# Optimization experiments

Hardware: AMD Instinct MI355X
Metric: run time of the kernel (lower is better)

Reference implementation:

```python
import jax, jax.numpy as jnp
import numpy as np

NH, NL, NPNT = 8, 4, 4          # heads, levels, points
NQ, BS, NK, D, DFFN = 100, 8, 18, 256, 1024
SPATIAL = np.array([[92, 92], [46, 46], [23, 23], [12, 12]], np.int32)
LEN_MEM = int((SPATIAL[:, 0] * SPATIAL[:, 1]).sum())  # 11253


def _layernorm(x, g, b):
    m = x.mean(-1, keepdims=True)
    v = ((x - m) ** 2).mean(-1, keepdims=True)
    return (x - m) / jnp.sqrt(v + 1e-5) * g + b


def _mha(xq, xk, xv, in_w, in_b, out_w, out_b):
    # torch nn.MultiheadAttention semantics, inputs (S, B, D)
    S, B, d = xq.shape
    dh = d // NH
    wq, wk, wv = jnp.split(in_w, 3, axis=0)
    bq, bk, bv = jnp.split(in_b, 3, axis=0)
    def proj(x, w, b):
        return (x @ w.T + b).reshape(x.shape[0], B, NH, dh).transpose(1, 2, 0, 3)
    q = proj(xq, wq, bq) * (1.0 / np.sqrt(dh))
    k = proj(xk, wk, bk)
    v = proj(xv, wv, bv)
    att = jax.nn.softmax(jnp.einsum('bhqd,bhkd->bhqk', q, k), axis=-1)
    o = jnp.einsum('bhqk,bhkd->bhqd', att, v).transpose(2, 0, 1, 3).reshape(S, B, d)
    return o @ out_w.T + out_b


def _bilinear(v_l, loc):
    # v_l: (bs,H,W,NH,dh); loc: (bs,Lq,NH,P,2) normalized [0,1]
    # matches F.grid_sample(align_corners=False, padding_mode='zeros')
    bs, H, W, nh, dh = v_l.shape
    x = loc[..., 0] * W - 0.5
    y = loc[..., 1] * H - 0.5
    x0 = jnp.floor(x); y0 = jnp.floor(y)
    lx = x - x0; ly = y - y0
    b_idx = jnp.arange(bs)[:, None, None, None]
    h_idx = jnp.arange(nh)[None, None, :, None]
    def corner(xa, ya, w):
        valid = (xa >= 0) & (xa < W) & (ya >= 0) & (ya < H)
        xi = jnp.clip(xa, 0, W - 1).astype(jnp.int32)
        yi = jnp.clip(ya, 0, H - 1).astype(jnp.int32)
        return v_l[b_idx, yi, xi, h_idx] * (w * valid)[..., None]
    return (corner(x0, y0, (1 - lx) * (1 - ly)) + corner(x0 + 1, y0, lx * (1 - ly))
            + corner(x0, y0 + 1, (1 - lx) * ly) + corner(x0 + 1, y0 + 1, lx * ly))


def _msda(q, rp, mem, pad_mask, ss, off_w, off_b, aw_w, aw_b, val_w, val_b, outp_w, outp_b):
    bs, Lq, d = q.shape
    dh = d // NH
    value = mem @ val_w.T + val_b
    value = jnp.where(pad_mask[..., None], 0.0, value).reshape(bs, -1, NH, dh)
    off = (q @ off_w.T + off_b).reshape(bs, Lq, NH, NL, NPNT, 2)
    aw = jax.nn.softmax((q @ aw_w.T + aw_b).reshape(bs, Lq, NH, NL * NPNT), -1)
    aw = aw.reshape(bs, Lq, NH, NL, NPNT)
    wh = jnp.asarray(ss[:, ::-1].copy(), jnp.float32)  # offset normalizer (W, H)
    loc = rp[:, :, None, :, None, :] + off / wh[None, None, None, :, None, :]
    out = jnp.zeros((bs, Lq, NH, dh), q.dtype)
    start = 0
    for l in range(NL):
        H, W = int(ss[l, 0]), int(ss[l, 1])
        v_l = value[:, start:start + H * W].reshape(bs, H, W, NH, dh)
        start += H * W
        samp = _bilinear(v_l, loc[:, :, :, l])          # (bs,Lq,NH,P,dh)
        out = out + (samp * aw[:, :, :, l, :, None]).sum(3)
    return out.reshape(bs, Lq, d) @ outp_w.T + outp_b


def _forward(tgt_pose, pos, ref_points, memory, w_in_w, w_in_b, w_out_w, w_out_b,
             a_in_w, a_in_b, a_out_w, a_out_b, off_w, off_b, aw_w, aw_b,
             val_w, val_b, outp_w, outp_b, wn_g, wn_b, an_g, an_b,
             n1_g, n1_b, n2_g, n2_b, l1_w, l1_b, l2_w, l2_b,
             spatial_shapes, level_start_index, padding_mask):
    ss = np.asarray(jax.device_get(spatial_shapes))
    nq, bs, nk, d = tgt_pose.shape
    # within-group self-attn over the nk keypoint tokens.
    # NOTE: with_pos_embed mutates tgt_pose in place in the torch code, so
    # q = k = v = tgt + pos and the residual also uses tgt + pos (faithful).
    t = tgt_pose + pos
    x = t.reshape(nq * bs, nk, d).transpose(1, 0, 2)   # (nk, nq*bs, d)
    a1 = _mha(x, x, x, w_in_w, w_in_b, w_out_w, w_out_b)
    t = _layernorm(t + a1.transpose(1, 0, 2).reshape(nq, bs, nk, d), wn_g, wn_b)
    # across-group self-attn over the nq groups
    x2 = t.reshape(nq, bs * nk, d)
    a2 = _mha(x2, x2, x2, a_in_w, a_in_b, a_out_w, a_out_b)
    t = _layernorm(t + a2.reshape(nq, bs, nk, d), an_g, an_b)
    # MSDeformAttn cross-attention (in-place pos add again, faithful)
    t = t + pos
    q = t.transpose(1, 0, 2, 3).reshape(bs, nq * nk, d)
    rp = jnp.swapaxes(ref_points, 0, 1)                # (bs, nq*nk, NL, 2)
    mem = jnp.swapaxes(memory, 0, 1)                   # (bs, LEN_MEM, d)
    c = _msda(q, rp, mem, padding_mask, ss, off_w, off_b, aw_w, aw_b,
              val_w, val_b, outp_w, outp_b)
    c = c.reshape(bs, nq, nk, d).transpose(1, 0, 2, 3)
    t = _layernorm(t + c, n1_g, n1_b)
    # FFN (dropout is identity in eval)
    h = jax.nn.relu(t @ l1_w.T + l1_b)
    return _layernorm(t + (h @ l2_w.T + l2_b), n2_g, n2_b)


def setup_inputs() -> dict:
    key = jax.random.key(0)
    ks = jax.random.split(key, 16)
    p = lambda k, shape: jax.random.normal(k, shape, jnp.float32) * 0.02
    lsi = np.concatenate([[0], np.cumsum(SPATIAL[:, 0] * SPATIAL[:, 1])[:-1]]).astype(np.int32)
    return {
        'tgt_pose': jax.random.normal(ks[0], (NQ, BS, NK, D), jnp.float32),
        'pos': jax.random.normal(ks[1], (NQ, BS, NK, D), jnp.float32),
        'ref_points': jax.random.uniform(ks[2], (NQ * NK, BS, NL, 2), jnp.float32),
        'memory': jax.random.normal(ks[3], (LEN_MEM, BS, D), jnp.float32),
        'w_in_w': p(ks[4], (3 * D, D)), 'w_in_b': jnp.zeros((3 * D,)),
        'w_out_w': p(ks[5], (D, D)), 'w_out_b': jnp.zeros((D,)),
        'a_in_w': p(ks[6], (3 * D, D)), 'a_in_b': jnp.zeros((3 * D,)),
        'a_out_w': p(ks[7], (D, D)), 'a_out_b': jnp.zeros((D,)),
        'off_w': p(ks[8], (NH * NL * NPNT * 2, D)),
        'off_b': jax.random.uniform(ks[9], (NH * NL * NPNT * 2,), jnp.float32, -2.0, 2.0),
        'aw_w': p(ks[10], (NH * NL * NPNT, D)), 'aw_b': jnp.zeros((NH * NL * NPNT,)),
        'val_w': p(ks[11], (D, D)), 'val_b': jnp.zeros((D,)),
        'outp_w': p(ks[12], (D, D)), 'outp_b': jnp.zeros((D,)),
        'wn_g': jnp.ones((D,)), 'wn_b': jnp.zeros((D,)),
        'an_g': jnp.ones((D,)), 'an_b': jnp.zeros((D,)),
        'n1_g': jnp.ones((D,)), 'n1_b': jnp.zeros((D,)),
        'n2_g': jnp.ones((D,)), 'n2_b': jnp.zeros((D,)),
        'l1_w': p(ks[13], (DFFN, D)), 'l1_b': jnp.zeros((DFFN,)),
        'l2_w': p(ks[14], (D, DFFN)), 'l2_b': jnp.zeros((D,)),
        'spatial_shapes': jnp.asarray(SPATIAL),
        'level_start_index': jnp.asarray(lsi),
        'padding_mask': jnp.zeros((BS, LEN_MEM), bool),
    }


def reference(tgt_pose, pos, ref_points, memory, w_in_w, w_in_b, w_out_w, w_out_b,
              a_in_w, a_in_b, a_out_w, a_out_b, off_w, off_b, aw_w, aw_b,
              val_w, val_b, outp_w, outp_b, wn_g, wn_b, an_g, an_b,
              n1_g, n1_b, n2_g, n2_b, l1_w, l1_b, l2_w, l2_b,
              spatial_shapes, level_start_index, padding_mask):
    return _forward(tgt_pose, pos, ref_points, memory, w_in_w, w_in_b, w_out_w, w_out_b,
                    a_in_w, a_in_b, a_out_w, a_out_b, off_w, off_b, aw_w, aw_b,
                    val_w, val_b, outp_w, outp_b, wn_g, wn_b, an_g, an_b,
                    n1_g, n1_b, n2_g, n2_b, l1_w, l1_b, l2_w, l2_b,
                    spatial_shapes, level_start_index, padding_mask)
```

## Files before the change

kernel.cpp:

```cpp
#include <hip/hip_runtime.h>
#include <math.h>

#define NH_ 8
#define D_ 256
#define NK_ 18
#define NQ_ 100
#define BS_ 8
#define LQ_ 1800
#define LEN_MEM_ 11253
#define NTOK_ 14400

typedef short bf16x8 __attribute__((ext_vector_type(8)));
typedef float f32x4 __attribute__((ext_vector_type(4)));
typedef unsigned short ushort;

__device__ inline ushort f2bf(float f) {
    unsigned int u = __builtin_bit_cast(unsigned int, f);
    unsigned int r = (u + 0x7fffu + ((u >> 16) & 1u)) >> 16;
    return (ushort)r;
}
__device__ inline float bf2f(unsigned int u16) {
    unsigned int i = u16 << 16;
    return __builtin_bit_cast(float, i);
}
__device__ inline float bf2f_hi(unsigned int u) {
    unsigned int i = u & 0xffff0000u;
    return __builtin_bit_cast(float, i);
}
__device__ inline float bf2f_lo(unsigned int u) {
    unsigned int i = u << 16;
    return __builtin_bit_cast(float, i);
}
__device__ inline int packbf2(float a, float b) {
    return (int)f2bf(a) | ((int)f2bf(b) << 16);
}

__global__ __launch_bounds__(256)
void wcvt_kernel(const float* s0, const float* s1, const float* s2, const float* s3,
                 const float* s4, const float* s5, const float* s6, const float* s7,
                 const float* s8, const float* s9, ushort* dst) {
    const int sizes[10] = {196608,65536,196608,65536,65536,32768,65536,65536,262144,262144};
    const int offs[10]  = {0,196608,262144,458752,524288,589824,622592,688128,753664,1015808};
    int ti = blockIdx.y;
    const float* s;
    switch (ti) {
        case 0: s = s0; break; case 1: s = s1; break; case 2: s = s2; break;
        case 3: s = s3; break; case 4: s = s4; break; case 5: s = s5; break;
        case 6: s = s6; break; case 7: s = s7; break; case 8: s = s8; break;
        default: s = s9; break;
    }
    int n = sizes[ti];
    int i = (blockIdx.x * 256 + threadIdx.x) * 8;
    if (i >= n) return;
    ushort* d = dst + offs[ti] + i;
    float4 f0 = *(const float4*)(s + i);
    float4 f1 = *(const float4*)(s + i + 4);
    int4 val;
    val.x = packbf2(f0.x, f0.y);
    val.y = packbf2(f0.z, f0.w);
    val.z = packbf2(f1.x, f1.y);
    val.w = packbf2(f1.z, f1.w);
    *(int4*)d = val;
}

__global__ __launch_bounds__(256)
void addcvt_kernel(const float* __restrict__ a, const float* __restrict__ b,
                   float* __restrict__ c, ushort* __restrict__ cbf, int n4) {
    int i = blockIdx.x * blockDim.x + threadIdx.x;
    if (i >= n4) return;
    float4 av = ((const float4*)a)[i];
    float4 bv = ((const float4*)b)[i];
    float4 cv;
    cv.x = av.x + bv.x; cv.y = av.y + bv.y; cv.z = av.z + bv.z; cv.w = av.w + bv.w;
    ((float4*)c)[i] = cv;
    uint2 p;
    p.x = (unsigned int)packbf2(cv.x, cv.y);
    p.y = (unsigned int)packbf2(cv.z, cv.w);
    *(uint2*)(cbf + (size_t)i * 4) = p;
}

template<int MODE, bool RELU, bool A_F32, bool OUT_BF16, int BN, int WAVES, int R>
__global__ __launch_bounds__(WAVES * 64)
void gemmw_kernel(const void* __restrict__ Av, const ushort* __restrict__ W,
                  const float* __restrict__ bias, void* __restrict__ Cv,
                  int M, int N, const unsigned char* __restrict__ mask) {
    constexpr int K = 256;
    constexpr int NT = BN / 16;
    __shared__ ushort Ws[32 * BN * 8];
    const int tid = threadIdx.x;
    const int m0 = blockIdx.x * (WAVES * 16 * R);
    const int n0 = blockIdx.y * BN;

    for (int c = tid; c < 32 * BN; c += WAVES * 64) {
        int kc = c & 31, n = c >> 5;
        int dst = kc * BN + (n ^ (kc & 7));
        *(int4*)(Ws + dst * 8) = *(const int4*)(W + (long)(n0 + n) * K + kc * 8);
    }
    __syncthreads();

    const int wv = tid >> 6, lane = tid & 63, fr = lane & 15, hi = lane >> 4;
    const int wm0 = m0 + wv * (16 * R);
    long arow[R];
#pragma unroll
    for (int r = 0; r < R; ++r) {
        int gr = wm0 + r * 16 + fr;
        if (gr > M - 1) gr = M - 1;
        if (MODE == 2) {
            int b = gr / LQ_; int lq = gr - b * LQ_;
            int q = lq / NK_; int kk = lq - q * NK_;
            arow[r] = (long)q * (BS_ * NK_) + b * NK_ + kk;
        } else {
            arow[r] = gr;
        }
    }

    f32x4 acc[R][NT];
#pragma unroll
    for (int r = 0; r < R; ++r)
#pragma unroll
        for (int t = 0; t < NT; ++t) acc[r][t] = f32x4{0.f, 0.f, 0.f, 0.f};

    if (A_F32) {
        const float* ap[R];
        float4 p0[R], p1[R];
#pragma unroll
        for (int r = 0; r < R; ++r) {
            ap[r] = (const float*)Av + arow[r] * (long)K + hi * 8;
            p0[r] = *(const float4*)ap[r];
            p1[r] = *(const float4*)(ap[r] + 4);
        }
#pragma unroll
        for (int ks = 0; ks < 8; ++ks) {
            bf16x8 cur[R];
#pragma unroll
            for (int r = 0; r < R; ++r) {
                int4 v;
                v.x = packbf2(p0[r].x, p0[r].y); v.y = packbf2(p0[r].z, p0[r].w);
                v.z = packbf2(p1[r].x, p1[r].y); v.w = packbf2(p1[r].z, p1[r].w);
                cur[r] = __builtin_bit_cast(bf16x8, v);
                if (ks < 7) {
                    p0[r] = *(const float4*)(ap[r] + (ks + 1) * 32);
                    p1[r] = *(const float4*)(ap[r] + (ks + 1) * 32 + 4);
                }
            }
            const int kc = ks * 4 + hi;
            const ushort* wb = Ws + ((kc * BN) + (fr ^ (kc & 7))) * 8;
#pragma unroll
            for (int t = 0; t < NT; ++t) {
                bf16x8 wf = *(const bf16x8*)(wb + t * 128);
#pragma unroll
                for (int r = 0; r < R; ++r)
                    acc[r][t] = __builtin_amdgcn_mfma_f32_16x16x32_bf16(cur[r], wf, acc[r][t], 0, 0, 0);
            }
        }
    } else {
        const ushort* ap[R];
        bf16x8 afrag[R];
#pragma unroll
        for (int r = 0; r < R; ++r) {
            ap[r] = (const ushort*)Av + arow[r] * (long)K + hi * 8;
            afrag[r] = *(const bf16x8*)ap[r];
        }
#pragma unroll
        for (int ks = 0; ks < 8; ++ks) {
            bf16x8 cur[R];
#pragma unroll
            for (int r = 0; r < R; ++r) {
                cur[r] = afrag[r];
                if (ks < 7) afrag[r] = *(const bf16x8*)(ap[r] + (ks + 1) * 32);
            }
            const int kc = ks * 4 + hi;
            const ushort* wb = Ws + ((kc * BN) + (fr ^ (kc & 7))) * 8;
#pragma unroll
            for (int t = 0; t < NT; ++t) {
                bf16x8 wf = *(const bf16x8*)(wb + t * 128);
#pragma unroll
                for (int r = 0; r < R; ++r)
                    acc[r][t] = __builtin_amdgcn_mfma_f32_16x16x32_bf16(cur[r], wf, acc[r][t], 0, 0, 0);
            }
        }
    }

#pragma unroll
    for (int r = 0; r < R; ++r) {
#pragma unroll
        for (int rr = 0; rr < 4; ++rr) {
            int gm = wm0 + r * 16 + hi * 4 + rr;
            if (gm >= M) continue;
            long orow = gm;
            bool zero = false;
            if (MODE == 1) {
                if (mask && mask[(size_t)(gm & 7) * LEN_MEM_ + (gm >> 3)]) zero = true;
            } else if (MODE == 3) {
                int b = gm / LQ_; int lq = gm - b * LQ_;
                int q = lq / NK_; int kk = lq - q * NK_;
                orow = (long)q * (BS_ * NK_) + b * NK_ + kk;
            }
#pragma unroll
            for (int t = 0; t < NT; ++t) {
                int gn = n0 + t * 16 + fr;
                float v = acc[r][t][rr] + bias[gn];
                if (RELU) v = fmaxf(v, 0.f);
                if (zero) v = 0.f;
                if (OUT_BF16) ((ushort*)Cv)[orow * (long)N + gn] = f2bf(v);
                else ((float*)Cv)[orow * (long)N + gn] = v;
            }
        }
    }
}

template<int MODE, bool RELU, bool A_F32, bool OUT_BF16>
__global__ __launch_bounds__(256)
void gemm_kernel(const void* __restrict__ Av, const ushort* __restrict__ W,
                 const float* __restrict__ bias, void* __restrict__ Cv,
                 int M, int N, int K, const unsigned char* __restrict__ mask) {
    constexpr int AST = 72;
    __shared__ ushort As[128 * AST];
    __shared__ ushort Bs[128 * AST];
    const int m0 = blockIdx.x * 128, n0 = blockIdx.y * 128;
    const int tid = threadIdx.x;
    const int w = tid >> 6, lane = tid & 63;
    const int wr = w >> 1, wc = w & 1;
    const int fr = lane & 15, hi = lane >> 4;
    f32x4 acc[4][4];
#pragma unroll
    for (int i = 0; i < 4; ++i)
#pragma unroll
        for (int j = 0; j < 4; ++j) acc[i][j] = f32x4{0.f, 0.f, 0.f, 0.f};

    const int srow = tid >> 1, shalf = tid & 1;
    long arow = 0;
    const bool avalid = (m0 + srow) < M;
    {
        int gr = m0 + srow;
        if (gr >= M) gr = M - 1;
        arow = gr;
    }

    for (int k0 = 0; k0 < K; k0 += 64) {
        ushort* ad = As + srow * AST + shalf * 32;
        if (avalid) {
            const ushort* ap = (const ushort*)Av + arow * (long)K + k0 + shalf * 32;
#pragma unroll
            for (int i = 0; i < 4; ++i) *(int4*)(ad + i * 8) = *(const int4*)(ap + i * 8);
        } else {
            int4 z = make_int4(0, 0, 0, 0);
#pragma unroll
            for (int i = 0; i < 4; ++i) *(int4*)(ad + i * 8) = z;
        }
        {
            const ushort* wp = W + (long)(n0 + srow) * K + k0 + shalf * 32;
            ushort* bd = Bs + srow * AST + shalf * 32;
#pragma unroll
            for (int i = 0; i < 4; ++i) *(int4*)(bd + i * 8) = *(const int4*)(wp + i * 8);
        }
        __syncthreads();
#pragma unroll
        for (int kb = 0; kb < 2; ++kb) {
            bf16x8 af[4], bfr[4];
#pragma unroll
            for (int i = 0; i < 4; ++i)
                af[i] = *(const bf16x8*)(As + (wr * 64 + i * 16 + fr) * AST + kb * 32 + hi * 8);
#pragma unroll
            for (int j = 0; j < 4; ++j)
                bfr[j] = *(const bf16x8*)(Bs + (wc * 64 + j * 16 + fr) * AST + kb * 32 + hi * 8);
#pragma unroll
            for (int i = 0; i < 4; ++i)
#pragma unroll
                for (int j = 0; j < 4; ++j)
                    acc[i][j] = __builtin_amdgcn_mfma_f32_16x16x32_bf16(af[i], bfr[j], acc[i][j], 0, 0, 0);
        }
        __syncthreads();
    }

#pragma unroll
    for (int i = 0; i < 4; ++i) {
#pragma unroll
        for (int r = 0; r < 4; ++r) {
            int gm = m0 + wr * 64 + i * 16 + hi * 4 + r;
            if (gm >= M) continue;
#pragma unroll
            for (int j = 0; j < 4; ++j) {
                int gn = n0 + wc * 64 + j * 16 + fr;
                float v = acc[i][j][r] + bias[gn];
                if (RELU) v = fmaxf(v, 0.f);
                if (OUT_BF16) ((ushort*)Cv)[(long)gm * N + gn] = f2bf(v);
                else ((float*)Cv)[(long)gm * N + gn] = v;
            }
        }
    }
}

template<int S, int SP, int HPB>
__global__ __launch_bounds__(256)
void mattn_kernel(const ushort* __restrict__ qkv, ushort* __restrict__ outb,
                  int rsG, int rsS) {
    constexpr int SPk = ((SP + 31) / 32) * 32;
    constexpr int KST = 40;
    constexpr int PST = SPk + 8;
    constexpr int NT = SP / 16;
    constexpr int NB = HPB * NT;
    constexpr int HB = 8 / HPB;
    __shared__ ushort KsA[HPB * SP * KST];
    __shared__ ushort VtA[HPB * 32 * PST];
    __shared__ ushort PA [HPB * SP * PST];

    const int tid = threadIdx.x;
    const int g = blockIdx.x / HB;
    const int hbase = (blockIdx.x % HB) * HPB;

    for (int idx = tid; idx < HPB * S * 4; idx += 256) {
        int hh = idx / (S * 4); int rem = idx - hh * (S * 4);
        int j = rem >> 2, q = rem & 3;
        const ushort* base = qkv + ((size_t)g * rsG + (size_t)j * rsS) * 768 + (hbase + hh) * 32 + q * 8;
        uint4 kv = *(const uint4*)(base + 256);
        ushort* kd = KsA + hh * (SP * KST) + j * KST + q * 8;
        *(uint2*)kd = make_uint2(kv.x, kv.y);
        *(uint2*)(kd + 4) = make_uint2(kv.z, kv.w);
        uint4 vv = *(const uint4*)(base + 512);
        ushort* vt = VtA + hh * (32 * PST) + j;
        unsigned int uu[4] = {vv.x, vv.y, vv.z, vv.w};
#pragma unroll
        for (int e = 0; e < 4; ++e) {
            vt[(q * 8 + e * 2    ) * PST] = (ushort)(uu[e] & 0xffff);
            vt[(q * 8 + e * 2 + 1) * PST] = (ushort)(uu[e] >> 16);
        }
    }
    for (int idx = tid; idx < HPB * 32 * (SPk - S); idx += 256) {
        int hh = idx / (32 * (SPk - S)); int rem = idx - hh * (32 * (SPk - S));
        int d = rem / (SPk - S); int c = S + rem - d * (SPk - S);
        VtA[hh * 32 * PST + d * PST + c] = 0;
    }
    if constexpr (SPk > SP) {
        constexpr int PW = SPk - SP;
        for (int idx = tid; idx < HPB * SP * PW; idx += 256) {
            int hh = idx / (SP * PW); int rem = idx - hh * (SP * PW);
            int rrow = rem / PW; int c = SP + rem - rrow * PW;
            PA[hh * SP * PST + rrow * PST + c] = 0;
        }
    }
    __syncthreads();

    const int wv = tid >> 6, lane = tid & 63, fr = lane & 15, hi = lane >> 4;
    for (int band = wv; band < NB; band += 4) {
        const int hh = band / NT, mb = band - (band / NT) * NT;
        const int h = hbase + hh;
        const ushort* Ks = KsA + hh * (SP * KST);
        const ushort* Vt = VtA + hh * (32 * PST);
        ushort* P = PA + hh * (SP * PST);

        int sq = mb * 16 + fr; if (sq > S - 1) sq = S - 1;
        bf16x8 qf = *(const bf16x8*)(qkv + ((size_t)g * rsG + (size_t)sq * rsS) * 768 + h * 32 + hi * 8);
        f32x4 sc[NT];
#pragma unroll
        for (int t = 0; t < NT; ++t) {
            bf16x8 kf = *(const bf16x8*)(Ks + (t * 16 + fr) * KST + hi * 8);
            sc[t] = __builtin_amdgcn_mfma_f32_16x16x32_bf16(qf, kf, f32x4{0.f, 0.f, 0.f, 0.f}, 0, 0, 0);
        }
#pragma unroll
        for (int t = 0; t < NT; ++t) {
            bool valid = (t * 16 + fr) < S;
#pragma unroll
            for (int r = 0; r < 4; ++r)
                sc[t][r] = valid ? sc[t][r] * 0.17677669529663687f : -1e30f;
        }
#pragma unroll
        for (int r = 0; r < 4; ++r) {
            float m = sc[0][r];
#pragma unroll
            for (int t = 1; t < NT; ++t) m = fmaxf(m, sc[t][r]);
            m = fmaxf(m, __shfl_xor(m, 1)); m = fmaxf(m, __shfl_xor(m, 2));
            m = fmaxf(m, __shfl_xor(m, 4)); m = fmaxf(m, __shfl_xor(m, 8));
            float e[NT]; float sum = 0.f;
#pragma unroll
            for (int t = 0; t < NT; ++t) { e[t] = __expf(sc[t][r] - m); sum += e[t]; }
            sum += __shfl_xor(sum, 1); sum += __shfl_xor(sum, 2);
            sum += __shfl_xor(sum, 4); sum += __shfl_xor(sum, 8);
            float inv = 1.f / sum;
            int row = mb * 16 + hi * 4 + r;
#pragma unroll
            for (int t = 0; t < NT; ++t)
                P[row * PST + t * 16 + fr] = f2bf(e[t] * inv);
        }
        f32x4 o0 = {0.f, 0.f, 0.f, 0.f}, o1 = {0.f, 0.f, 0.f, 0.f};
#pragma unroll
        for (int kb = 0; kb < SPk / 32; ++kb) {
            bf16x8 pf = *(const bf16x8*)(P + (mb * 16 + fr) * PST + kb * 32 + hi * 8);
            bf16x8 v0 = *(const bf16x8*)(Vt + fr * PST + kb * 32 + hi * 8);
            bf16x8 v1 = *(const bf16x8*)(Vt + (16 + fr) * PST + kb * 32 + hi * 8);
            o0 = __builtin_amdgcn_mfma_f32_16x16x32_bf16(pf, v0, o0, 0, 0, 0);
            o1 = __builtin_amdgcn_mfma_f32_16x16x32_bf16(pf, v1, o1, 0, 0, 0);
        }
#pragma unroll
        for (int r = 0; r < 4; ++r) {
            int s = mb * 16 + hi * 4 + r;
            if (s < S) {
                size_t ob = ((size_t)g * rsG + (size_t)s * rsS) * 256 + h * 32;
                outb[ob + fr] = f2bf(o0[r]);
                outb[ob + 16 + fr] = f2bf(o1[r]);
            }
        }
    }
}

__global__ __launch_bounds__(256)
void addln_kernel(const float* __restrict__ base, const float* __restrict__ delta,
                  const float* __restrict__ gamma, const float* __restrict__ beta,
                  const float* __restrict__ pos,
                  float* __restrict__ out, ushort* __restrict__ obf, int M) {
    int row = blockIdx.x * 4 + (threadIdx.x >> 6);
    int lane = threadIdx.x & 63;
    if (row >= M) return;
    const float* pb = base + (size_t)row * 256;
    const float* pd = delta + (size_t)row * 256;
    float v[4]; float s = 0.f;
#pragma unroll
    for (int i = 0; i < 4; ++i) { int c = lane + i * 64; v[i] = pb[c] + pd[c]; s += v[i]; }
#pragma unroll
    for (int off = 32; off; off >>= 1) s += __shfl_xor(s, off);
    float mean = s * (1.f / 256.f);
    float var = 0.f;
#pragma unroll
    for (int i = 0; i < 4; ++i) { float d = v[i] - mean; var += d * d; }
#pragma unroll
    for (int off = 32; off; off >>= 1) var += __shfl_xor(var, off);
    var *= (1.f / 256.f);
    float rstd = rsqrtf(var + 1e-5f);
#pragma unroll
    for (int i = 0; i < 4; ++i) {
        int c = lane + i * 64;
        float o = (v[i] - mean) * rstd * gamma[c] + beta[c];
        if (pos) o += pos[(size_t)row * 256 + c];
        out[(size_t)row * 256 + c] = o;
        if (obf) obf[(size_t)row * 256 + c] = f2bf(o);
    }
}

__global__ __launch_bounds__(256)
void msda_kernel(const float* __restrict__ offb, const float* __restrict__ aw,
                 const ushort* __restrict__ val, const float* __restrict__ refp,
                 const int* __restrict__ spatial, const int* __restrict__ lsi,
                 ushort* __restrict__ samp) {
    const int unit = blockIdx.x * 64 + (threadIdx.x >> 2);
    const int lane4 = threadIdx.x & 3;
    const int base = (threadIdx.x & 63) & 60;
    const int h = unit & 7;
    const int t = unit >> 3;
    const int lq = t % LQ_;
    const int b = t / LQ_;
    const size_t row = (size_t)b * LQ_ + lq;

    float4 lg = *(const float4*)(aw + row * 128 + h * 16 + lane4 * 4);
    float m = fmaxf(fmaxf(lg.x, lg.y), fmaxf(lg.z, lg.w));
    m = fmaxf(m, __shfl_xor(m, 1)); m = fmaxf(m, __shfl_xor(m, 2));
    float4 e;
    e.x = __expf(lg.x - m); e.y = __expf(lg.y - m);
    e.z = __expf(lg.z - m); e.w = __expf(lg.w - m);
    float s = e.x + e.y + e.z + e.w;
    s += __shfl_xor(s, 1); s += __shfl_xor(s, 2);
    float inv = 1.f / s;
    float4 w4; w4.x = e.x * inv; w4.y = e.y * inv; w4.z = e.z * inv; w4.w = e.w * inv;

    const float* offp = offb + row * 256 + h * 32;
    float4 oA = *(const float4*)(offp + lane4 * 8);
    float4 oB = *(const float4*)(offp + lane4 * 8 + 4);

    float acc[8];
#pragma unroll
    for (int c = 0; c < 8; ++c) acc[c] = 0.f;

#pragma unroll
    for (int lvl = 0; lvl < 4; ++lvl) {
        int H = spatial[lvl * 2], W = spatial[lvl * 2 + 1];
        int st = lsi[lvl];
        float rpx = refp[(((size_t)lq * BS_ + b) * 4 + lvl) * 2 + 0];
        float rpy = refp[(((size_t)lq * BS_ + b) * 4 + lvl) * 2 + 1];
        const ushort* vb = val + ((size_t)st * 8 + b) * 256 + h * 32 + lane4 * 8;
        float fW = (float)W, fH = (float)H;
#pragma unroll
        for (int p = 0; p < 4; ++p) {
            const int pi = lvl * 4 + p;
            const int j = pi >> 2, q = pi & 3;
            float ox_, oy_, wp_;
            if (q == 0)      { ox_ = oA.x; oy_ = oA.y; wp_ = w4.x; }
            else if (q == 1) { ox_ = oA.z; oy_ = oA.w; wp_ = w4.y; }
            else if (q == 2) { ox_ = oB.x; oy_ = oB.y; wp_ = w4.z; }
            else             { ox_ = oB.z; oy_ = oB.w; wp_ = w4.w; }
            float ox  = __shfl(ox_, base + j);
            float oy  = __shfl(oy_, base + j);
            float wpt = __shfl(wp_, base + j);

            float x = rpx * fW + ox - 0.5f;
            float y = rpy * fH + oy - 0.5f;
            float x0f = floorf(x), y0f = floorf(y);
            float lx = x - x0f, ly = y - y0f;
            int x0 = (int)x0f, y0 = (int)y0f;
            int xc0 = min(max(x0, 0), W - 1), xc1 = min(max(x0 + 1, 0), W - 1);
            int yc0 = min(max(y0, 0), H - 1), yc1 = min(max(y0 + 1, 0), H - 1);
            float vx0 = (x0 >= 0 && x0 < W) ? 1.f : 0.f;
            float vx1 = (x0 >= -1 && x0 + 1 < W) ? 1.f : 0.f;
            float vy0 = (y0 >= 0 && y0 < H) ? 1.f : 0.f;
            float vy1 = (y0 >= -1 && y0 + 1 < H) ? 1.f : 0.f;
            float w00 = wpt * (1.f - lx) * (1.f - ly) * vx0 * vy0;
            float w10 = wpt * lx * (1.f - ly) * vx1 * vy0;
            float w01 = wpt * (1.f - lx) * ly * vx0 * vy1;
            float w11 = wpt * lx * ly * vx1 * vy1;
            uint4 u00 = *(const uint4*)(vb + (size_t)(yc0 * W + xc0) * 2048);
            uint4 u10 = *(const uint4*)(vb + (size_t)(yc0 * W + xc1) * 2048);
            uint4 u01 = *(const uint4*)(vb + (size_t)(yc1 * W + xc0) * 2048);
            uint4 u11 = *(const uint4*)(vb + (size_t)(yc1 * W + xc1) * 2048);
            const unsigned int* a00 = (const unsigned int*)&u00;
            const unsigned int* a10 = (const unsigned int*)&u10;
            const unsigned int* a01 = (const unsigned int*)&u01;
            const unsigned int* a11 = (const unsigned int*)&u11;
#pragma unroll
            for (int k = 0; k < 4; ++k) {
                acc[2 * k]     += w00 * bf2f_lo(a00[k]) + w10 * bf2f_lo(a10[k])
                                + w01 * bf2f_lo(a01[k]) + w11 * bf2f_lo(a11[k]);
                acc[2 * k + 1] += w00 * bf2f_hi(a00[k]) + w10 * bf2f_hi(a10[k])
                                + w01 * bf2f_hi(a01[k]) + w11 * bf2f_hi(a11[k]);
            }
        }
    }
    size_t o = row * 256 + h * 32 + lane4 * 8;
    uint4 pk;
    pk.x = (unsigned int)packbf2(acc[0], acc[1]);
    pk.y = (unsigned int)packbf2(acc[2], acc[3]);
    pk.z = (unsigned int)packbf2(acc[4], acc[5]);
    pk.w = (unsigned int)packbf2(acc[6], acc[7]);
    *(uint4*)(samp + o) = pk;
}

extern "C" void kernel_launch(void* const* d_in, const int* in_sizes, int n_in,
                              void* d_out, int out_size, void* d_ws, size_t ws_size,
                              hipStream_t stream) {
    const float* tgt     = (const float*)d_in[0];
    const float* pos     = (const float*)d_in[1];
    const float* refp    = (const float*)d_in[2];
    const float* memory  = (const float*)d_in[3];
    const float* w_in_w  = (const float*)d_in[4];
    const float* w_in_b  = (const float*)d_in[5];
    const float* w_out_w = (const float*)d_in[6];
    const float* w_out_b = (const float*)d_in[7];
    const float* a_in_w  = (const float*)d_in[8];
    const float* a_in_b  = (const float*)d_in[9];
    const float* a_out_w = (const float*)d_in[10];
    const float* a_out_b = (const float*)d_in[11];
    const float* off_w   = (const float*)d_in[12];
    const float* off_b   = (const float*)d_in[13];
    const float* aw_w    = (const float*)d_in[14];
    const float* aw_b    = (const float*)d_in[15];
    const float* val_w   = (const float*)d_in[16];
    const float* val_b   = (const float*)d_in[17];
    const float* outp_w  = (const float*)d_in[18];
    const float* outp_b  = (const float*)d_in[19];
    const float* wn_g    = (const float*)d_in[20];
    const float* wn_b    = (const float*)d_in[21];
    const float* an_g    = (const float*)d_in[22];
    const float* an_b    = (const float*)d_in[23];
    const float* n1_g    = (const float*)d_in[24];
    const float* n1_b    = (const float*)d_in[25];
    const float* n2_g    = (const float*)d_in[26];
    const float* n2_b    = (const float*)d_in[27];
    const float* l1_w    = (const float*)d_in[28];
    const float* l1_b    = (const float*)d_in[29];
    const float* l2_w    = (const float*)d_in[30];
    const float* l2_b    = (const float*)d_in[31];
    const int*   spatial = (const int*)d_in[32];
    const int*   lsi     = (const int*)d_in[33];
    const unsigned char* pmask = (const unsigned char*)d_in[34];
    float* out = (float*)d_out;

    float*  T      = (float*)d_ws;
    ushort* Tbf    = (ushort*)(T + 3686400);
    ushort* B16    = Tbf + 3686400;
    ushort* CBbf   = B16 + 11059200;
    ushort* VALbf  = CBbf + 3686400;
    ushort* SAMPbf = VALbf + 23046144;
    ushort* Hbf    = SAMPbf + 3686400;
    ushort* WB     = Hbf + 14745600;
    float*  OFF    = (float*)(WB + 1277952);
    float*  AW     = OFF + 3686400;

    ushort* WB_win  = WB + 0;
    ushort* WB_wout = WB + 196608;
    ushort* WB_ain  = WB + 262144;
    ushort* WB_aout = WB + 458752;
    ushort* WB_off  = WB + 524288;
    ushort* WB_aw   = WB + 589824;
    ushort* WB_val  = WB + 622592;
    ushort* WB_outp = WB + 688128;
    ushort* WB_l1   = WB + 753664;
    ushort* WB_l2   = WB + 1015808;

    const int n4 = NTOK_ * 256 / 4;

    wcvt_kernel<<<dim3(128, 10), 256, 0, stream>>>(
        w_in_w, w_out_w, a_in_w, a_out_w, off_w, aw_w, val_w, outp_w, l1_w, l2_w, WB);
    addcvt_kernel<<<n4 / 256, 256, 0, stream>>>(tgt, pos, T, Tbf, n4);
    gemmw_kernel<0, false, false, true, 64, 4, 2><<<dim3(113, 12), 256, 0, stream>>>(
        Tbf, WB_win, w_in_b, B16, NTOK_, 768, nullptr);
    mattn_kernel<18, 32, 4><<<800 * 2, 256, 0, stream>>>(B16, CBbf, 18, 1);
    gemmw_kernel<0, false, false, false, 64, 4, 2><<<dim3(113, 4), 256, 0, stream>>>(
        CBbf, WB_wout, w_out_b, OFF, NTOK_, 256, nullptr);
    addln_kernel<<<NTOK_ / 4, 256, 0, stream>>>(T, OFF, wn_g, wn_b, nullptr, T, Tbf, NTOK_);
    gemmw_kernel<0, false, false, true, 64, 4, 2><<<dim3(113, 12), 256, 0, stream>>>(
        Tbf, WB_ain, a_in_b, B16, NTOK_, 768, nullptr);
    mattn_kernel<100, 112, 1><<<144 * 8, 256, 0, stream>>>(B16, CBbf, 1, 144);
    gemmw_kernel<0, false, false, false, 64, 4, 2><<<dim3(113, 4), 256, 0, stream>>>(
        CBbf, WB_aout, a_out_b, OFF, NTOK_, 256, nullptr);
    addln_kernel<<<NTOK_ / 4, 256, 0, stream>>>(T, OFF, an_g, an_b, pos, T, Tbf, NTOK_);
    gemmw_kernel<1, false, true, true, 128, 8, 2><<<dim3(352, 2), 512, 0, stream>>>(
        memory, WB_val, val_b, VALbf, 90024, 256, pmask);
    gemmw_kernel<2, false, false, false, 64, 4, 2><<<dim3(113, 4), 256, 0, stream>>>(
        Tbf, WB_off, off_b, OFF, NTOK_, 256, nullptr);
    gemmw_kernel<2, false, false, false, 64, 4, 2><<<dim3(113, 2), 256, 0, stream>>>(
        Tbf, WB_aw, aw_b, AW, NTOK_, 128, nullptr);
    msda_kernel<<<1800, 256, 0, stream>>>(OFF, AW, VALbf, refp, spatial, lsi, SAMPbf);
    gemmw_kernel<3, false, false, false, 64, 4, 2><<<dim3(113, 4), 256, 0, stream>>>(
        SAMPbf, WB_outp, outp_b, OFF, NTOK_, 256, nullptr);
    addln_kernel<<<NTOK_ / 4, 256, 0, stream>>>(T, OFF, n1_g, n1_b, nullptr, T, Tbf, NTOK_);
    gemmw_kernel<0, true, false, true, 64, 4, 2><<<dim3(113, 16), 256, 0, stream>>>(
        Tbf, WB_l1, l1_b, Hbf, NTOK_, 1024, nullptr);
    gemm_kernel<0, false, false, false><<<dim3(113, 2), 256, 0, stream>>>(
        Hbf, WB_l2, l2_b, OFF, NTOK_, 256, 1024, nullptr);
    addln_kernel<<<NTOK_ / 4, 256, 0, stream>>>(T, OFF, n2_g, n2_b, nullptr, out, nullptr, NTOK_);
}
```

Measured before the change: 359.6 us.

## Stage fp32 value-projection A tile through LDS with coalesced loads

Adds a dedicated value-projection GEMM that loads a 128-row fp32 memory tile with fully coalesced float4 reads, converts it to bf16 once, and stores it swizzled in LDS before the MFMA loop. It replaces the previous path where each lane streamed strided fp32 fragments straight from global memory, and removes the now-unused fp32-A branch from the generic GEMM. It is aimed at the memory-bound value projection over 90k rows. In exchange it uses more LDS per block (about 128 KB), which limits occupancy to one block per CU, and it launches twice as many blocks with one row tile per wave.

```diff
diff --git a/kernel.cpp b/kernel.cpp
--- a/kernel.cpp
+++ b/kernel.cpp
@@ -79,6 +79,74 @@
     *(uint2*)(cbf + (size_t)i * 4) = p;
 }
 
+__global__ __launch_bounds__(512)
+void gemmv_kernel(const float* __restrict__ A, const ushort* __restrict__ W,
+                  const float* __restrict__ bias, ushort* __restrict__ C,
+                  int M, int N, const unsigned char* __restrict__ mask) {
+    constexpr int K = 256;
+    constexpr int BN = 128;
+    __shared__ ushort Ws[32 * BN * 8];
+    __shared__ ushort As[32 * 128 * 8];
+    const int tid = threadIdx.x;
+    const int m0 = blockIdx.x * 128;
+    const int n0 = blockIdx.y * BN;
+
+    for (int c = tid; c < 32 * BN; c += 512) {
+        int kc = c & 31, n = c >> 5;
+        int dst = kc * BN + (n ^ (kc & 7));
+        *(int4*)(Ws + dst * 8) = *(const int4*)(W + (long)(n0 + n) * K + kc * 8);
+    }
+    {
+        const float4* src = (const float4*)(A + (size_t)m0 * K);
+#pragma unroll
+        for (int s = 0; s < 16; ++s) {
+            int p4 = s * 512 + tid;
+            int row = p4 >> 6;
+            int p4r = (m0 + row < M) ? p4 : (p4 & 63);
+            float4 f = src[p4r];
+            int k8 = (p4 >> 1) & 31, half = p4 & 1;
+            uint2 v;
+            v.x = (unsigned int)packbf2(f.x, f.y);
+            v.y = (unsigned int)packbf2(f.z, f.w);
+            *(uint2*)(As + (k8 * 128 + (row ^ (k8 & 7))) * 8 + half * 4) = v;
+        }
+    }
+    __syncthreads();
+
+    const int wv = tid >> 6, lane = tid & 63, fr = lane & 15, hi = lane >> 4;
+    const int rowl = wv * 16 + fr;
+
+    f32x4 acc[8];
+#pragma unroll
+    for (int t = 0; t < 8; ++t) acc[t] = f32x4{0.f, 0.f, 0.f, 0.f};
+
+#pragma unroll
+    for (int ks = 0; ks < 8; ++ks) {
+        const int kc = ks * 4 + hi;
+        bf16x8 af = *(const bf16x8*)(As + (kc * 128 + (rowl ^ (kc & 7))) * 8);
+        const ushort* wb = Ws + ((kc * BN) + (fr ^ (kc & 7))) * 8;
+#pragma unroll
+        for (int t = 0; t < 8; ++t) {
+            bf16x8 wf = *(const bf16x8*)(wb + t * 128);
+            acc[t] = __builtin_amdgcn_mfma_f32_16x16x32_bf16(af, wf, acc[t], 0, 0, 0);
+        }
+    }
+
+#pragma unroll
+    for (int rr = 0; rr < 4; ++rr) {
+        int gm = m0 + wv * 16 + hi * 4 + rr;
+        if (gm >= M) continue;
+        bool zero = mask && mask[(size_t)(gm & 7) * LEN_MEM_ + (gm >> 3)];
+#pragma unroll
+        for (int t = 0; t < 8; ++t) {
+            int gn = n0 + t * 16 + fr;
+            float v = acc[t][rr] + bias[gn];
+            if (zero) v = 0.f;
+            C[(long)gm * N + gn] = f2bf(v);
+        }
+    }
+}
+
 template<int MODE, bool RELU, bool A_F32, bool OUT_BF16, int BN, int WAVES, int R>
 __global__ __launch_bounds__(WAVES * 64)
 void gemmw_kernel(const void* __restrict__ Av, const ushort* __restrict__ W,
@@ -120,40 +188,7 @@
 #pragma unroll
         for (int t = 0; t < NT; ++t) acc[r][t] = f32x4{0.f, 0.f, 0.f, 0.f};
 
-    if (A_F32) {
-        const float* ap[R];
-        float4 p0[R], p1[R];
-#pragma unroll
-        for (int r = 0; r < R; ++r) {
-            ap[r] = (const float*)Av + arow[r] * (long)K + hi * 8;
-            p0[r] = *(const float4*)ap[r];
-            p1[r] = *(const float4*)(ap[r] + 4);
-        }
-#pragma unroll
-        for (int ks = 0; ks < 8; ++ks) {
-            bf16x8 cur[R];
-#pragma unroll
-            for (int r = 0; r < R; ++r) {
-                int4 v;
-                v.x = packbf2(p0[r].x, p0[r].y); v.y = packbf2(p0[r].z, p0[r].w);
-                v.z = packbf2(p1[r].x, p1[r].y); v.w = packbf2(p1[r].z, p1[r].w);
-                cur[r] = __builtin_bit_cast(bf16x8, v);
-                if (ks < 7) {
-                    p0[r] = *(const float4*)(ap[r] + (ks + 1) * 32);
-                    p1[r] = *(const float4*)(ap[r] + (ks + 1) * 32 + 4);
-                }
-            }
-            const int kc = ks * 4 + hi;
-            const ushort* wb = Ws + ((kc * BN) + (fr ^ (kc & 7))) * 8;
-#pragma unroll
-            for (int t = 0; t < NT; ++t) {
-                bf16x8 wf = *(const bf16x8*)(wb + t * 128);
-#pragma unroll
-                for (int r = 0; r < R; ++r)
-                    acc[r][t] = __builtin_amdgcn_mfma_f32_16x16x32_bf16(cur[r], wf, acc[r][t], 0, 0, 0);
-            }
-        }
-    } else {
+    {
         const ushort* ap[R];
         bf16x8 afrag[R];
 #pragma unroll
@@ -610,7 +645,7 @@
     gemmw_kernel<0, false, false, false, 64, 4, 2><<<dim3(113, 4), 256, 0, stream>>>(
         CBbf, WB_aout, a_out_b, OFF, NTOK_, 256, nullptr);
     addln_kernel<<<NTOK_ / 4, 256, 0, stream>>>(T, OFF, an_g, an_b, pos, T, Tbf, NTOK_);
-    gemmw_kernel<1, false, true, true, 128, 8, 2><<<dim3(352, 2), 512, 0, stream>>>(
+    gemmv_kernel<<<dim3(704, 2), 512, 0, stream>>>(
         memory, WB_val, val_b, VALbf, 90024, 256, pmask);
     gemmw_kernel<2, false, false, false, 64, 4, 2><<<dim3(113, 4), 256, 0, stream>>>(
         Tbf, WB_off, off_b, OFF, NTOK_, 256, nullptr);
```

After: 376.2 us. 1.05x slower.
